# Kernel optimization log

Measured on AMD Instinct MI355X. Metric: run time of the kernel, lower is better.

## Reference

```python
import jax, jax.numpy as jnp
import numpy as np

N = 6144      # nodes
IN = 512      # input_dim
D = 256       # HIDDEN_DIM (out_features per head)
H = 1         # HEADS
OUT = 128     # OUT_DIM
ALPHA = 0.2   # LeakyReLU slope
EPS = 1e-5    # LayerNorm eps


def _xavier(k, shape):
    fan_in, fan_out = shape[-2], shape[-1]
    lim = float(np.sqrt(6.0 / (fan_in + fan_out)))
    return jax.random.uniform(k, shape, jnp.float32, -lim, lim)


def _gat(x, W, a_src, a_dst, adj):
    # x: [N, IN], W: [IN, H*D], a_src/a_dst: [H, D], adj: [N, N] int
    n = x.shape[0]
    h = (x @ W).reshape(n, H, D)                       # [N, H, D]
    e1 = jnp.einsum('nhd,hd->nh', h, a_src)            # src score
    e2 = jnp.einsum('nhd,hd->nh', h, a_dst)            # dst score
    e = jax.nn.leaky_relu(e1[:, None, :] + e2[None, :, :], ALPHA)  # [N, N, H]
    e = jnp.where(adj[:, :, None] > 0, e, jnp.float32(-1e9))
    att = jnp.nan_to_num(jax.nn.softmax(e, axis=1), nan=0.0)       # softmax over dim -2 (j)
    out = jnp.einsum('nbh,bhd->nhd', att, h)           # weighted aggregation over j
    return out.reshape(n, H * D)                       # is_concat=True


def _ln(x, g, b):
    m = jnp.mean(x, axis=-1, keepdims=True)
    v = jnp.mean((x - m) ** 2, axis=-1, keepdims=True)
    return (x - m) * jax.lax.rsqrt(v + EPS) * g + b


def setup_inputs() -> dict:
    key = jax.random.key(0)
    ks = jax.random.split(key, 20)
    inp = {
        'x': jax.random.normal(ks[0], (N, IN), jnp.float32),
        'adj_cf': jax.random.randint(ks[1], (N, N), 0, 2, jnp.int32),
        'adj_org': jax.random.randint(ks[2], (N, N), 0, 2, jnp.int32),
        'adj_per': jax.random.randint(ks[3], (N, N), 0, 2, jnp.int32),
        'W_cf': _xavier(ks[4], (IN, H * D)),
        'a_src_cf': _xavier(ks[5], (H, D)),
        'a_dst_cf': _xavier(ks[6], (H, D)),
        'W_org': _xavier(ks[7], (IN, H * D)),
        'a_src_org': _xavier(ks[8], (H, D)),
        'a_dst_org': _xavier(ks[9], (H, D)),
        'W_per': _xavier(ks[10], (IN, H * D)),
        'a_src_per': _xavier(ks[11], (H, D)),
        'a_dst_per': _xavier(ks[12], (H, D)),
        'proj_W': _xavier(ks[13], (H * D, OUT)),
        'proj_b': jnp.zeros((OUT,), jnp.float32),
        'ln_g': jnp.ones((OUT,), jnp.float32),
        'ln_b': jnp.zeros((OUT,), jnp.float32),
        'alpha': jnp.ones((3, 1), jnp.float32),
    }
    return inp


def reference(x, adj_cf, adj_org, adj_per,
              W_cf, a_src_cf, a_dst_cf,
              W_org, a_src_org, a_dst_org,
              W_per, a_src_per, a_dst_per,
              proj_W, proj_b, ln_g, ln_b, alpha):
    # dropout layers are identity in eval mode
    h_cf = _gat(x, W_cf, a_src_cf, a_dst_cf, adj_cf)
    h_org = _gat(x, W_org, a_src_org, a_dst_org, adj_org)
    h_per = _gat(x, W_per, a_src_per, a_dst_per, adj_per)
    z_cf = _ln(h_cf @ proj_W + proj_b, ln_g, ln_b)
    z_org = _ln(h_org @ proj_W + proj_b, ln_g, ln_b)
    z_per = _ln(h_per @ proj_W + proj_b, ln_g, ln_b)
    w = jax.nn.softmax(alpha, axis=0)                  # [3, 1]
    z = w[0] * z_cf + w[1] * z_org + w[2] * z_per
    z = jnp.nan_to_num(z, nan=0.0, posinf=0.0, neginf=0.0)
    return (z, w)
```

## Files before the change

kernel.cpp:

```cpp
#include <hip/hip_runtime.h>

typedef _Float16 half_t;
typedef _Float16 f16x8 __attribute__((ext_vector_type(8)));
typedef _Float16 f16x4 __attribute__((ext_vector_type(4)));
typedef float f32x4 __attribute__((ext_vector_type(4)));
typedef unsigned long long u64;

#define NN 6144
#define IN_DIM 512
#define DD 256
#define OUT_DIM 128
#define SPLIT 4
#define JT 24
#define LOG2E 1.44269504088896340736f

__device__ __forceinline__ f32x4 mfma16(f16x8 a, f16x8 b, f32x4 c) {
  return __builtin_amdgcn_mfma_f32_16x16x32_f16(a, b, c, 0, 0, 0);
}

__global__ void cvt_x_kernel(const float* __restrict__ x, half_t* __restrict__ xh) {
  int idx = (blockIdx.x * 256 + threadIdx.x) * 4;
  float4 v = *(const float4*)(x + idx);
  f16x4 h;
  h[0] = (half_t)v.x; h[1] = (half_t)v.y; h[2] = (half_t)v.z; h[3] = (half_t)v.w;
  *(f16x4*)(xh + idx) = h;
}

__global__ void cvt_w_kernel(const float* __restrict__ W0, const float* __restrict__ W1,
                             const float* __restrict__ W2, const float* __restrict__ pW,
                             half_t* __restrict__ WT, half_t* __restrict__ pWT) {
  int y = blockIdx.y;
  int idx = blockIdx.x * 256 + threadIdx.x;
  if (y < 3) {
    const float* W = (y == 0) ? W0 : (y == 1) ? W1 : W2;
    int k = idx >> 8, n = idx & 255;
    WT[(size_t)y * DD * IN_DIM + (size_t)n * IN_DIM + k] = (half_t)W[idx];
  } else if (idx < DD * OUT_DIM) {
    int k = idx >> 7, o = idx & 127;
    pWT[(size_t)o * DD + k] = (half_t)pW[idx];
  }
}

__global__ __launch_bounds__(256, 2) void gemm1_kernel(
    const half_t* __restrict__ xh, const half_t* __restrict__ WT,
    const float* __restrict__ as0, const float* __restrict__ as1, const float* __restrict__ as2,
    const float* __restrict__ ad0, const float* __restrict__ ad1, const float* __restrict__ ad2,
    half_t* __restrict__ hT, float* __restrict__ e1, float* __restrict__ e2) {
  int v = blockIdx.y;
  int i0 = blockIdx.x * 64;
  int t = threadIdx.x;
  int lane = t & 63, w = t >> 6;
  int lr = lane & 15, lg = lane >> 4;
  const half_t* Wv = WT + (size_t)v * DD * IN_DIM;
  const float* asv = (v == 0) ? as0 : (v == 1) ? as1 : as2;
  const float* adv = (v == 0) ? ad0 : (v == 1) ? ad1 : ad2;
  f32x4 acc[4][4] = {};
  for (int kt = 0; kt < 16; ++kt) {
    int k = kt * 32 + lg * 8;
    f16x8 af[4], bf[4];
#pragma unroll
    for (int mf = 0; mf < 4; ++mf)
      af[mf] = *(const f16x8*)(xh + (size_t)(i0 + mf * 16 + lr) * IN_DIM + k);
#pragma unroll
    for (int nf = 0; nf < 4; ++nf)
      bf[nf] = *(const f16x8*)(Wv + (size_t)(w * 64 + nf * 16 + lr) * IN_DIM + k);
#pragma unroll
    for (int mf = 0; mf < 4; ++mf)
#pragma unroll
      for (int nf = 0; nf < 4; ++nf)
        acc[mf][nf] = mfma16(af[mf], bf[nf], acc[mf][nf]);
  }
  __shared__ half_t tr[4][64 * 64];
  __shared__ float ep1[4][64], ep2[4][64];
  char* trw = (char*)tr[w];
#pragma unroll
  for (int mf = 0; mf < 4; ++mf)
#pragma unroll
    for (int nf = 0; nf < 4; ++nf)
#pragma unroll
      for (int r = 0; r < 4; ++r) {
        int dl = nf * 16 + lr;
        int il = mf * 16 + lg * 4 + r;
        unsigned addr = (unsigned)((dl * 128 + il * 2) ^ ((dl & 7) << 4));
        *(half_t*)(trw + addr) = (half_t)acc[mf][nf][r];
      }
  float as_c[4], ad_c[4];
#pragma unroll
  for (int nf = 0; nf < 4; ++nf) {
    int col = w * 64 + nf * 16 + lr;
    as_c[nf] = asv[col];
    ad_c[nf] = adv[col];
  }
#pragma unroll
  for (int mf = 0; mf < 4; ++mf)
#pragma unroll
    for (int r = 0; r < 4; ++r) {
      float p1 = 0.f, p2 = 0.f;
#pragma unroll
      for (int nf = 0; nf < 4; ++nf) {
        p1 = fmaf(acc[mf][nf][r], as_c[nf], p1);
        p2 = fmaf(acc[mf][nf][r], ad_c[nf], p2);
      }
      p1 += __shfl_xor(p1, 1); p1 += __shfl_xor(p1, 2);
      p1 += __shfl_xor(p1, 4); p1 += __shfl_xor(p1, 8);
      p2 += __shfl_xor(p2, 1); p2 += __shfl_xor(p2, 2);
      p2 += __shfl_xor(p2, 4); p2 += __shfl_xor(p2, 8);
      if (lr == 0) {
        int il = mf * 16 + lg * 4 + r;
        ep1[w][il] = p1;
        ep2[w][il] = p2;
      }
    }
  __syncthreads();
  half_t* hTv = hT + (size_t)v * DD * NN;
#pragma unroll
  for (int c = 0; c < 8; ++c) {
    unsigned addr = (unsigned)((lane * 128 + c * 16) ^ ((lane & 7) << 4));
    f16x8 val = *(const f16x8*)(trw + addr);
    *(f16x8*)(hTv + (size_t)(w * 64 + lane) * NN + i0 + c * 8) = val;
  }
  if (t < 64) {
    e1[v * NN + i0 + t] = LOG2E * (ep1[0][t] + ep1[1][t] + ep1[2][t] + ep1[3][t]);
    e2[v * NN + i0 + t] = LOG2E * (ep2[0][t] + ep2[1][t] + ep2[2][t] + ep2[3][t]);
  }
}

__global__ void e2max_kernel(const float* __restrict__ e2, float* __restrict__ e2m) {
  int v = blockIdx.x;
  __shared__ float red[256];
  float m = -1e30f;
  for (int i = threadIdx.x; i < NN; i += 256) m = fmaxf(m, e2[v * NN + i]);
  red[threadIdx.x] = m;
  __syncthreads();
  for (int s = 128; s > 0; s >>= 1) {
    if (threadIdx.x < s) red[threadIdx.x] = fmaxf(red[threadIdx.x], red[threadIdx.x + s]);
    __syncthreads();
  }
  if (threadIdx.x == 0) e2m[v] = red[0];
}

__global__ __launch_bounds__(256, 2) void gat_kernel(
    const int* __restrict__ adj0, const int* __restrict__ adj1, const int* __restrict__ adj2,
    const half_t* __restrict__ hT,
    const float* __restrict__ e1g, const float* __restrict__ e2g,
    const float* __restrict__ e2maxg, half_t* __restrict__ pacc, float* __restrict__ pl) {
  int v = blockIdx.z, s = blockIdx.y;
  const int* __restrict__ adjv = (v == 0) ? adj0 : (v == 1) ? adj1 : adj2;
  int i0 = blockIdx.x * 64;
  int t = threadIdx.x;
  int lane = t & 63, w = t >> 6;
  int lr = lane & 15, lg = lane >> 4;
  int jq = t & 15, rg = t >> 4;

  __shared__ half_t hbuf0[DD * 64];
  __shared__ half_t hbuf1[DD * 64];
  __shared__ half_t P0[64 * 64];
  __shared__ half_t P1[64 * 64];

  const half_t* hTv = hT + (size_t)v * DD * NN;
  const float* e2v = e2g + v * NN;
  const int jbase = s * JT * 64;

  float e1r[4], mr[4];
  float e2mL = e2maxg[v];
#pragma unroll
  for (int it = 0; it < 4; ++it) {
    float e1i = e1g[v * NN + i0 + it * 16 + rg];
    e1r[it] = e1i;
    float sm = e1i + e2mL;
    mr[it] = fmaxf(sm, 0.2f * sm);
  }

  f32x4 acc[4][4] = {};
  float lpart[4] = {0.f, 0.f, 0.f, 0.f};

  int sub = lane >> 3;
  int c_src = (lane & 7) ^ sub;
  auto gload = [&](half_t* hb, int jt) {
    int j0 = jbase + jt * 64;
#pragma unroll
    for (int q = 0; q < 8; ++q) {
      const half_t* gp = hTv + (size_t)(w * 64 + q * 8 + sub) * NN + j0 + c_src * 8;
      half_t* lp = hb + (w * 8 + q) * 512;
      __builtin_amdgcn_global_load_lds(
          (const __attribute__((address_space(1))) int*)gp,
          (__attribute__((address_space(3))) int*)lp, 16, 0, 0);
    }
  };
  auto load_adj = [&](int4 (&aw)[4], int jt) {
    int j0 = jbase + jt * 64;
#pragma unroll
    for (int it = 0; it < 4; ++it)
      aw[it] = *(const int4*)(adjv + (size_t)(i0 + it * 16 + rg) * NN + j0 + jq * 4);
  };
  auto comp_p = [&](const int4 (&aw)[4], const float4& e2q, char* pb) {
    float e2a[4] = {e2q.x, e2q.y, e2q.z, e2q.w};
#pragma unroll
    for (int it = 0; it < 4; ++it) {
      int il = it * 16 + rg;
      int a4[4] = {aw[it].x, aw[it].y, aw[it].z, aw[it].w};
      f16x4 ph;
      float ssum = 0.f;
#pragma unroll
      for (int c = 0; c < 4; ++c) {
        float s1 = e1r[it] + e2a[c];
        float u = fmaxf(s1, 0.2f * s1) - mr[it];
        float p = (a4[c] > 0) ? exp2f(u) : 0.f;
        ssum += p;
        ph[c] = (half_t)p;
      }
      lpart[it] += ssum;
      unsigned addr = (unsigned)((il * 128 + jq * 8) ^ ((il & 7) << 4));
      *(f16x4*)(pb + addr) = ph;
    }
  };
  auto do_mfma = [&](const char* pb, const half_t* hb) {
#pragma unroll
    for (int kf = 0; kf < 2; ++kf) {
      f16x8 bfr[4];
#pragma unroll
      for (int nf = 0; nf < 4; ++nf) {
        int d = w * 64 + nf * 16 + lr;
        unsigned ba = (unsigned)(d * 128 + ((kf * 64 + lg * 16) ^ ((lr & 7) << 4)));
        bfr[nf] = *(const f16x8*)((const char*)hb + ba);
      }
#pragma unroll
      for (int mf = 0; mf < 4; ++mf) {
        int row = mf * 16 + lr;
        unsigned pa = (unsigned)((row * 128 + kf * 64 + lg * 16) ^ ((row & 7) << 4));
        f16x8 af = *(const f16x8*)(pb + pa);
#pragma unroll
        for (int nf = 0; nf < 4; ++nf)
          acc[mf][nf] = mfma16(af, bfr[nf], acc[mf][nf]);
      }
    }
  };

  int4 awA[4], awB[4];
  float4 e2A, e2B;

  load_adj(awA, 0);
  e2A = *(const float4*)(e2v + jbase + jq * 4);
  gload(hbuf0, 0);
  __syncthreads();

  for (int tt = 0; tt < JT; tt += 2) {
    comp_p(awA, e2A, (char*)P0);
    __syncthreads();
    {
      load_adj(awB, tt + 1);
      e2B = *(const float4*)(e2v + jbase + (tt + 1) * 64 + jq * 4);
      gload(hbuf1, tt + 1);
    }
    do_mfma((char*)P0, hbuf0);

    comp_p(awB, e2B, (char*)P1);
    __syncthreads();
    if (tt + 2 < JT) {
      load_adj(awA, tt + 2);
      e2A = *(const float4*)(e2v + jbase + (tt + 2) * 64 + jq * 4);
      gload(hbuf0, tt + 2);
    }
    do_mfma((char*)P1, hbuf1);
  }

  size_t sl = (size_t)v * SPLIT + s;
#pragma unroll
  for (int it = 0; it < 4; ++it) {
    float ssum = lpart[it];
    ssum += __shfl_xor(ssum, 1); ssum += __shfl_xor(ssum, 2);
    ssum += __shfl_xor(ssum, 4); ssum += __shfl_xor(ssum, 8);
    if (jq == 0) pl[sl * NN + i0 + it * 16 + rg] = ssum;
  }

  half_t* pa = pacc + sl * (size_t)NN * DD;
#pragma unroll
  for (int mf = 0; mf < 4; ++mf)
#pragma unroll
    for (int r = 0; r < 4; ++r) {
      int il = mf * 16 + lg * 4 + r;
#pragma unroll
      for (int nf = 0; nf < 4; ++nf)
        pa[(size_t)(i0 + il) * DD + w * 64 + nf * 16 + lr] = (half_t)acc[mf][nf][r];
    }
}

__global__ __launch_bounds__(64) void proj_kernel(
    const half_t* __restrict__ pacc, const float* __restrict__ pl,
    const half_t* __restrict__ pWT,
    const float* __restrict__ proj_b, const float* __restrict__ ln_g,
    const float* __restrict__ ln_b, const float* __restrict__ alpha,
    float* __restrict__ out) {
  int i0 = blockIdx.x * 16;
  int t = threadIdx.x;
  int lr = t & 15, lg = t >> 4;
  float a0 = alpha[0], a1 = alpha[1], a2 = alpha[2];
  float am = fmaxf(a0, fmaxf(a1, a2));
  float x0 = __expf(a0 - am), x1 = __expf(a1 - am), x2 = __expf(a2 - am);
  float inv = 1.f / (x0 + x1 + x2);
  float wv[3] = {x0 * inv, x1 * inv, x2 * inv};
  __shared__ float rlv[3][16];
  if (t < 48) {
    int v = t >> 4, i = t & 15;
    float l = 0.f;
#pragma unroll
    for (int s = 0; s < SPLIT; ++s)
      l += pl[((size_t)v * SPLIT + s) * NN + i0 + i];
    rlv[v][i] = (l > 0.f) ? 1.f / l : 0.f;
  }
  float pb[8], gg[8], bb[8];
#pragma unroll
  for (int nf = 0; nf < 8; ++nf) {
    pb[nf] = proj_b[nf * 16 + lr];
    gg[nf] = ln_g[nf * 16 + lr];
    bb[nf] = ln_b[nf * 16 + lr];
  }
  __syncthreads();
  f32x4 zacc[8] = {};
  for (int v = 0; v < 3; ++v) {
    float rl = rlv[v][lr];
    f32x4 yac[8] = {};
    const half_t* p0 = pacc + (((size_t)v * SPLIT + 0) * NN + i0 + lr) * DD;
    const half_t* p1 = pacc + (((size_t)v * SPLIT + 1) * NN + i0 + lr) * DD;
    const half_t* p2 = pacc + (((size_t)v * SPLIT + 2) * NN + i0 + lr) * DD;
    const half_t* p3 = pacc + (((size_t)v * SPLIT + 3) * NN + i0 + lr) * DD;
    for (int kt = 0; kt < 8; ++kt) {
      int k = kt * 32 + lg * 8;
      f16x8 s0 = *(const f16x8*)(p0 + k);
      f16x8 s1 = *(const f16x8*)(p1 + k);
      f16x8 s2 = *(const f16x8*)(p2 + k);
      f16x8 s3 = *(const f16x8*)(p3 + k);
      f16x8 af;
#pragma unroll
      for (int e = 0; e < 8; ++e)
        af[e] = (half_t)((((float)s0[e] + (float)s1[e]) +
                          ((float)s2[e] + (float)s3[e])) * rl);
#pragma unroll
      for (int nf = 0; nf < 8; ++nf) {
        f16x8 bf = *(const f16x8*)(pWT + (size_t)(nf * 16 + lr) * DD + k);
        yac[nf] = mfma16(af, bf, yac[nf]);
      }
    }
#pragma unroll
    for (int r = 0; r < 4; ++r) {
      float ssum = 0.f, q = 0.f;
#pragma unroll
      for (int nf = 0; nf < 8; ++nf) {
        float y = yac[nf][r] + pb[nf];
        yac[nf][r] = y;
        ssum += y; q += y * y;
      }
      ssum += __shfl_xor(ssum, 1); ssum += __shfl_xor(ssum, 2);
      ssum += __shfl_xor(ssum, 4); ssum += __shfl_xor(ssum, 8);
      q += __shfl_xor(q, 1); q += __shfl_xor(q, 2);
      q += __shfl_xor(q, 4); q += __shfl_xor(q, 8);
      float mean = ssum * (1.f / 128.f);
      float var = q * (1.f / 128.f) - mean * mean;
      float rstd = rsqrtf(var + 1e-5f);
      float wvv = wv[v];
#pragma unroll
      for (int nf = 0; nf < 8; ++nf)
        zacc[nf][r] += wvv * (yac[nf][r] - mean) * rstd;
    }
  }
#pragma unroll
  for (int nf = 0; nf < 8; ++nf)
#pragma unroll
    for (int r = 0; r < 4; ++r) {
      int row = i0 + lg * 4 + r;
      float z = zacc[nf][r] * gg[nf] + bb[nf];
      if (!isfinite(z)) z = 0.f;
      out[(size_t)row * OUT_DIM + nf * 16 + lr] = z;
    }
  if (blockIdx.x == 0 && t < 3) out[(size_t)NN * OUT_DIM + t] = wv[t];
}

extern "C" void kernel_launch(void* const* d_in, const int* in_sizes, int n_in,
                              void* d_out, int out_size, void* d_ws, size_t ws_size,
                              hipStream_t stream) {
  const float* x      = (const float*)d_in[0];
  const int*   adj_cf = (const int*)d_in[1];
  const int*   adj_or = (const int*)d_in[2];
  const int*   adj_pe = (const int*)d_in[3];
  const float* W_cf   = (const float*)d_in[4];
  const float* as_cf  = (const float*)d_in[5];
  const float* ad_cf  = (const float*)d_in[6];
  const float* W_or   = (const float*)d_in[7];
  const float* as_or  = (const float*)d_in[8];
  const float* ad_or  = (const float*)d_in[9];
  const float* W_pe   = (const float*)d_in[10];
  const float* as_pe  = (const float*)d_in[11];
  const float* ad_pe  = (const float*)d_in[12];
  const float* proj_W = (const float*)d_in[13];
  const float* proj_b = (const float*)d_in[14];
  const float* ln_g   = (const float*)d_in[15];
  const float* ln_b   = (const float*)d_in[16];
  const float* alpha  = (const float*)d_in[17];

  char* ws = (char*)d_ws;
  half_t* xh     = (half_t*)(ws + 0);
  half_t* WT     = (half_t*)(ws + 6291456);
  half_t* pWT    = (half_t*)(ws + 7077888);
  half_t* hT     = (half_t*)(ws + 7143424);
  float*  e1     = (float*)(ws + 16580608);
  float*  e2     = (float*)(ws + 16654336);
  float*  e2m    = (float*)(ws + 16728064);
  half_t* pacc   = (half_t*)(ws + 16728128);
  float*  pl     = (float*)(ws + 54476864);

  cvt_x_kernel<<<3072, 256, 0, stream>>>(x, xh);
  cvt_w_kernel<<<dim3(512, 4), 256, 0, stream>>>(W_cf, W_or, W_pe, proj_W, WT, pWT);
  gemm1_kernel<<<dim3(96, 3), 256, 0, stream>>>(xh, WT, as_cf, as_or, as_pe,
                                                ad_cf, ad_or, ad_pe, hT, e1, e2);
  e2max_kernel<<<3, 256, 0, stream>>>(e2, e2m);
  gat_kernel<<<dim3(96, SPLIT, 3), 256, 0, stream>>>(adj_cf, adj_or, adj_pe, hT,
                                                     e1, e2, e2m, pacc, pl);
  proj_kernel<<<384, 64, 0, stream>>>(pacc, pl, pWT, proj_b, ln_g, ln_b, alpha,
                                      (float*)d_out);
}
```

Before: 261.3 us.

## Widen GAT kernel to 512 threads with explicit waitcnt pipelining and triple-buffered adj

Doubles the GAT attention block to 8 waves, giving each wave half the output columns and half the P rows to compute. The main loop is replaced by a fully unrolled macro region that uses hand-placed lgkmcnt barriers and vmcnt waits, so the async global-to-LDS h loads and adjacency prefetches (now triple-buffered, two tiles ahead) overlap with the MFMA work. The intent is to hide memory latency and raise occupancy. The cost is fragile manual wait counts, more register pressure per wave at launch_bounds(512,4), and possible ordering hazards if the vmcnt values do not match the loads actually issued.

After: 512.4 us. +96.1%, slower.

```diff
diff --git a/kernel.cpp b/kernel.cpp
--- a/kernel.cpp
+++ b/kernel.cpp
@@ -17,6 +17,9 @@
 __device__ __forceinline__ f32x4 mfma16(f16x8 a, f16x8 b, f32x4 c) {
   return __builtin_amdgcn_mfma_f32_16x16x32_f16(a, b, c, 0, 0, 0);
 }
+
+#define LBAR() asm volatile("s_waitcnt lgkmcnt(0)\n\ts_barrier" ::: "memory")
+#define VWAIT(N) asm volatile("s_waitcnt vmcnt(" #N ")" ::: "memory")
 
 __global__ void cvt_x_kernel(const float* __restrict__ x, half_t* __restrict__ xh) {
   int idx = (blockIdx.x * 256 + threadIdx.x) * 4;
@@ -139,7 +142,7 @@
   if (threadIdx.x == 0) e2m[v] = red[0];
 }
 
-__global__ __launch_bounds__(256, 2) void gat_kernel(
+__global__ __launch_bounds__(512, 4) void gat_kernel(
     const int* __restrict__ adj0, const int* __restrict__ adj1, const int* __restrict__ adj2,
     const half_t* __restrict__ hT,
     const float* __restrict__ e1g, const float* __restrict__ e2g,
@@ -152,8 +155,8 @@
   int lr = lane & 15, lg = lane >> 4;
   int jq = t & 15, rg = t >> 4;
 
-  __shared__ half_t hbuf0[DD * 64];
-  __shared__ half_t hbuf1[DD * 64];
+  __shared__ half_t H0[DD * 64];
+  __shared__ half_t H1[DD * 64];
   __shared__ half_t P0[64 * 64];
   __shared__ half_t P1[64 * 64];
 
@@ -161,43 +164,42 @@
   const float* e2v = e2g + v * NN;
   const int jbase = s * JT * 64;
 
-  float e1r[4], mr[4];
+  float e1r[2], mr[2];
   float e2mL = e2maxg[v];
 #pragma unroll
-  for (int it = 0; it < 4; ++it) {
-    float e1i = e1g[v * NN + i0 + it * 16 + rg];
+  for (int it = 0; it < 2; ++it) {
+    float e1i = e1g[v * NN + i0 + it * 32 + rg];
     e1r[it] = e1i;
     float sm = e1i + e2mL;
     mr[it] = fmaxf(sm, 0.2f * sm);
   }
 
-  f32x4 acc[4][4] = {};
-  float lpart[4] = {0.f, 0.f, 0.f, 0.f};
+  f32x4 acc[4][2] = {};
+  float lpart[2] = {0.f, 0.f};
 
   int sub = lane >> 3;
   int c_src = (lane & 7) ^ sub;
   auto gload = [&](half_t* hb, int jt) {
     int j0 = jbase + jt * 64;
 #pragma unroll
-    for (int q = 0; q < 8; ++q) {
-      const half_t* gp = hTv + (size_t)(w * 64 + q * 8 + sub) * NN + j0 + c_src * 8;
-      half_t* lp = hb + (w * 8 + q) * 512;
+    for (int q = 0; q < 4; ++q) {
+      const half_t* gp = hTv + (size_t)(w * 32 + q * 8 + sub) * NN + j0 + c_src * 8;
+      half_t* lp = hb + (w * 32 + q * 8) * 64;
       __builtin_amdgcn_global_load_lds(
           (const __attribute__((address_space(1))) int*)gp,
           (__attribute__((address_space(3))) int*)lp, 16, 0, 0);
     }
   };
-  auto load_adj = [&](int4 (&aw)[4], int jt) {
+  auto load_adj = [&](int4 (&aw)[2], int jt) {
     int j0 = jbase + jt * 64;
-#pragma unroll
-    for (int it = 0; it < 4; ++it)
-      aw[it] = *(const int4*)(adjv + (size_t)(i0 + it * 16 + rg) * NN + j0 + jq * 4);
+    aw[0] = *(const int4*)(adjv + (size_t)(i0 + rg) * NN + j0 + jq * 4);
+    aw[1] = *(const int4*)(adjv + (size_t)(i0 + 32 + rg) * NN + j0 + jq * 4);
   };
-  auto comp_p = [&](const int4 (&aw)[4], const float4& e2q, char* pb) {
+  auto comp_p = [&](const int4 (&aw)[2], const float4& e2q, char* pb) {
     float e2a[4] = {e2q.x, e2q.y, e2q.z, e2q.w};
 #pragma unroll
-    for (int it = 0; it < 4; ++it) {
-      int il = it * 16 + rg;
+    for (int it = 0; it < 2; ++it) {
+      int il = it * 32 + rg;
       int a4[4] = {aw[it].x, aw[it].y, aw[it].z, aw[it].w};
       f16x4 ph;
       float ssum = 0.f;
@@ -217,60 +219,72 @@
   auto do_mfma = [&](const char* pb, const half_t* hb) {
 #pragma unroll
     for (int kf = 0; kf < 2; ++kf) {
-      f16x8 bfr[4];
-#pragma unroll
-      for (int nf = 0; nf < 4; ++nf) {
-        int d = w * 64 + nf * 16 + lr;
+      f16x8 bfr[2];
+#pragma unroll
+      for (int nf = 0; nf < 2; ++nf) {
+        int d = w * 32 + nf * 16 + lr;
         unsigned ba = (unsigned)(d * 128 + ((kf * 64 + lg * 16) ^ ((lr & 7) << 4)));
         bfr[nf] = *(const f16x8*)((const char*)hb + ba);
       }
 #pragma unroll
       for (int mf = 0; mf < 4; ++mf) {
         int row = mf * 16 + lr;
-        unsigned pa = (unsigned)((row * 128 + kf * 64 + lg * 16) ^ ((row & 7) << 4));
-        f16x8 af = *(const f16x8*)(pb + pa);
-#pragma unroll
-        for (int nf = 0; nf < 4; ++nf)
+        unsigned pa_ = (unsigned)((row * 128 + kf * 64 + lg * 16) ^ ((row & 7) << 4));
+        f16x8 af = *(const f16x8*)(pb + pa_);
+#pragma unroll
+        for (int nf = 0; nf < 2; ++nf)
           acc[mf][nf] = mfma16(af, bfr[nf], acc[mf][nf]);
       }
     }
   };
 
-  int4 awA[4], awB[4];
-  float4 e2A, e2B;
-
+  int4 awA[2], awB[2], awC[2];
+  float4 e2A, e2B, e2C;
+
+  gload(H0, 0);
   load_adj(awA, 0);
   e2A = *(const float4*)(e2v + jbase + jq * 4);
-  gload(hbuf0, 0);
-  __syncthreads();
-
-  for (int tt = 0; tt < JT; tt += 2) {
-    comp_p(awA, e2A, (char*)P0);
-    __syncthreads();
-    {
-      load_adj(awB, tt + 1);
-      e2B = *(const float4*)(e2v + jbase + (tt + 1) * 64 + jq * 4);
-      gload(hbuf1, tt + 1);
-    }
-    do_mfma((char*)P0, hbuf0);
-
-    comp_p(awB, e2B, (char*)P1);
-    __syncthreads();
-    if (tt + 2 < JT) {
-      load_adj(awA, tt + 2);
-      e2A = *(const float4*)(e2v + jbase + (tt + 2) * 64 + jq * 4);
-      gload(hbuf0, tt + 2);
-    }
-    do_mfma((char*)P1, hbuf1);
-  }
+  load_adj(awB, 1);
+  e2B = *(const float4*)(e2v + jbase + 64 + jq * 4);
+
+#define REGION(T, AWc, AWn, E2c, E2n, Pc, Hc, Hn, VN)                \
+  {                                                                  \
+    comp_p(AWc, E2c, (char*)(Pc));                                   \
+    LBAR();                                                          \
+    if ((T) + 1 < JT) gload(Hn, (T) + 1);                            \
+    if ((T) + 2 < JT) {                                              \
+      load_adj(AWn, (T) + 2);                                        \
+      E2n = *(const float4*)(e2v + jbase + ((T) + 2) * 64 + jq * 4); \
+    }                                                                \
+    __builtin_amdgcn_sched_barrier(0);                               \
+    VWAIT(VN);                                                       \
+    __builtin_amdgcn_sched_barrier(0);                               \
+    do_mfma((char*)(Pc), Hc);                                        \
+  }
+
+  for (int k = 0; k < 18; k += 6) {
+    REGION(k + 0, awA, awC, e2A, e2C, P0, H0, H1, 10);
+    REGION(k + 1, awB, awA, e2B, e2A, P1, H1, H0, 10);
+    REGION(k + 2, awC, awB, e2C, e2B, P0, H0, H1, 10);
+    REGION(k + 3, awA, awC, e2A, e2C, P1, H1, H0, 10);
+    REGION(k + 4, awB, awA, e2B, e2A, P0, H0, H1, 10);
+    REGION(k + 5, awC, awB, e2C, e2B, P1, H1, H0, 10);
+  }
+  REGION(18, awA, awC, e2A, e2C, P0, H0, H1, 10);
+  REGION(19, awB, awA, e2B, e2A, P1, H1, H0, 10);
+  REGION(20, awC, awB, e2C, e2B, P0, H0, H1, 10);
+  REGION(21, awA, awC, e2A, e2C, P1, H1, H0, 10);
+  REGION(22, awB, awA, e2B, e2A, P0, H0, H1, 7);
+  REGION(23, awC, awB, e2C, e2B, P1, H1, H0, 0);
+#undef REGION
 
   size_t sl = (size_t)v * SPLIT + s;
 #pragma unroll
-  for (int it = 0; it < 4; ++it) {
+  for (int it = 0; it < 2; ++it) {
     float ssum = lpart[it];
     ssum += __shfl_xor(ssum, 1); ssum += __shfl_xor(ssum, 2);
     ssum += __shfl_xor(ssum, 4); ssum += __shfl_xor(ssum, 8);
-    if (jq == 0) pl[sl * NN + i0 + it * 16 + rg] = ssum;
+    if (jq == 0) pl[sl * NN + i0 + it * 32 + rg] = ssum;
   }
 
   half_t* pa = pacc + sl * (size_t)NN * DD;
@@ -280,8 +294,8 @@
     for (int r = 0; r < 4; ++r) {
       int il = mf * 16 + lg * 4 + r;
 #pragma unroll
-      for (int nf = 0; nf < 4; ++nf)
-        pa[(size_t)(i0 + il) * DD + w * 64 + nf * 16 + lr] = (half_t)acc[mf][nf][r];
+      for (int nf = 0; nf < 2; ++nf)
+        pa[(size_t)(i0 + il) * DD + w * 32 + nf * 16 + lr] = (half_t)acc[mf][nf][r];
     }
 }
 
@@ -413,7 +427,7 @@
   gemm1_kernel<<<dim3(96, 3), 256, 0, stream>>>(xh, WT, as_cf, as_or, as_pe,
                                                 ad_cf, ad_or, ad_pe, hT, e1, e2);
   e2max_kernel<<<3, 256, 0, stream>>>(e2, e2m);
-  gat_kernel<<<dim3(96, SPLIT, 3), 256, 0, stream>>>(adj_cf, adj_or, adj_pe, hT,
+  gat_kernel<<<dim3(96, SPLIT, 3), 512, 0, stream>>>(adj_cf, adj_or, adj_pe, hT,
                                                      e1, e2, e2m, pacc, pl);
   proj_kernel<<<384, 64, 0, stream>>>(pacc, pl, pWT, proj_b, ln_g, ln_b, alpha,
                                       (float*)d_out);
```
